# Optimization experiments

Measured on AMD Instinct MI355X. Metric: run time of the kernel, lower is better.

The kernel has to match this reference:

```python
import jax, jax.numpy as jnp
import numpy as np

N_HEAD = 16
N_KV_GROUP = 4
WINDOW = 256


def setup_inputs() -> dict:
    key = jax.random.key(0)
    ks = jax.random.split(key, 5)
    B, T, C = 2, 2048, 1024
    KV = C // N_HEAD * N_KV_GROUP  # 256
    s = 0.02
    return {
        "x": jax.random.normal(ks[0], (B, T, C), jnp.float32),
        "Wq": jax.random.normal(ks[1], (C, C), jnp.float32) * s,
        "bq": jnp.zeros((C,), jnp.float32),
        "Wk": jax.random.normal(ks[2], (C, KV), jnp.float32) * s,
        "bk": jnp.zeros((KV,), jnp.float32),
        "Wv": jax.random.normal(ks[3], (C, KV), jnp.float32) * s,
        "bv": jnp.zeros((KV,), jnp.float32),
        "Wo": jax.random.normal(ks[4], (C, C), jnp.float32) * s,
        "bo": jnp.zeros((C,), jnp.float32),
    }


def reference(x, Wq, bq, Wk, bk, Wv, bv, Wo, bo):
    B, T, C = x.shape
    hd = C // N_HEAD  # head dim = 64
    n_rep = N_HEAD // N_KV_GROUP

    q = x @ Wq + bq                      # [B,T,C]
    k = x @ Wk + bk                      # [B,T,KV]
    v = x @ Wv + bv

    q = q.reshape(B, T, N_HEAD, hd).transpose(0, 2, 1, 3)       # [B,H,T,d]
    k = k.reshape(B, T, N_KV_GROUP, hd).transpose(0, 2, 1, 3)   # [B,G,T,d]
    v = v.reshape(B, T, N_KV_GROUP, hd).transpose(0, 2, 1, 3)

    # GQA: repeat_interleave kv heads along head dim
    k_rep = jnp.repeat(k, n_rep, axis=1)                         # [B,H,T,d]
    v_rep = jnp.repeat(v, n_rep, axis=1)

    att = jnp.einsum("bhqd,bhkd->bhqk", q, k_rep) / jnp.sqrt(jnp.float32(hd))

    # causal + sliding window band mask: q position i attends to j in [i-WINDOW, i]
    i = jnp.arange(T)[:, None]
    j = jnp.arange(T)[None, :]
    band = (j <= i) & (j >= i - WINDOW)                           # [T,T]
    att = jnp.where(band[None, None], att, jnp.float32(-jnp.inf))

    att = jax.nn.softmax(att, axis=-1)
    y = jnp.einsum("bhqk,bhkd->bhqd", att, v_rep)                 # [B,H,T,d]
    y = y.transpose(0, 2, 1, 3).reshape(B, T, C)
    return y @ Wo + bo
```

## Files before the change

kernel.cpp:

```cpp
#include <hip/hip_runtime.h>
#include <hip/hip_bf16.h>

#define TT 2048
#define CC 1024
#define KVD 256
#define QKVD 1536

typedef __bf16 bf16x8 __attribute__((ext_vector_type(8)));
typedef float f32x4 __attribute__((ext_vector_type(4)));

__device__ __forceinline__ void gload_lds16(const __hip_bfloat16* g, __hip_bfloat16* l) {
  __builtin_amdgcn_global_load_lds(
      (const __attribute__((address_space(1))) unsigned int*)g,
      (__attribute__((address_space(3))) unsigned int*)l, 16, 0, 0);
}


__global__ __launch_bounds__(256) void k_convert_x(const float* __restrict__ x,
                                                   __hip_bfloat16* __restrict__ xbf) {
  size_t idx = ((size_t)blockIdx.x * 256 + threadIdx.x) * 4;
  float4 v = *(const float4*)(x + idx);
  xbf[idx + 0] = __float2bfloat16(v.x);
  xbf[idx + 1] = __float2bfloat16(v.y);
  xbf[idx + 2] = __float2bfloat16(v.z);
  xbf[idx + 3] = __float2bfloat16(v.w);
}

__global__ __launch_bounds__(256) void k_pack_w(const float* __restrict__ Wq,
                                                const float* __restrict__ Wk,
                                                const float* __restrict__ Wv,
                                                const float* __restrict__ Wo,
                                                const float* __restrict__ bq,
                                                const float* __restrict__ bk,
                                                const float* __restrict__ bv,
                                                __hip_bfloat16* __restrict__ wqkvT,
                                                __hip_bfloat16* __restrict__ woT,
                                                float* __restrict__ bqkv) {
  if (blockIdx.z == 1 && blockIdx.y >= 16) {
    if (blockIdx.y == 16 && blockIdx.x == 0) {
      for (int i = threadIdx.x; i < 1536; i += 256) {
        float v;
        if (i < 1024)      v = bq[i];
        else if (i < 1280) v = bk[i - 1024];
        else               v = bv[i - 1280];
        bqkv[i] = v;
      }
    }
    return;
  }
  __shared__ float tile[64][65];
  const int k0 = blockIdx.x * 64;
  const int n0 = blockIdx.y * 64;
  const float* src;
  int ncols;
  __hip_bfloat16* dst;
  if (blockIdx.z == 0) {
    dst = wqkvT;
    if (n0 < 1024)      { src = Wq; ncols = 1024; }
    else if (n0 < 1280) { src = Wk - 1024; ncols = 256; }
    else                { src = Wv - 1280; ncols = 256; }
  } else {
    dst = woT; src = Wo; ncols = 1024;
  }
  const int rw = threadIdx.x >> 6;
  const int cl = threadIdx.x & 63;
#pragma unroll
  for (int i = 0; i < 16; ++i) {
    const int kr = rw + i * 4;
    tile[kr][cl] = src[(size_t)(k0 + kr) * ncols + n0 + cl];
  }
  __syncthreads();
#pragma unroll
  for (int i = 0; i < 16; ++i) {
    const int nr = rw + i * 4;
    dst[(size_t)(n0 + nr) * 1024 + k0 + cl] = __float2bfloat16(tile[cl][nr]);
  }
}

__global__ __launch_bounds__(256) void k_vT(const __hip_bfloat16* __restrict__ qkv,
                                            __hip_bfloat16* __restrict__ vtg) {
  __shared__ __hip_bfloat16 tile[64][72];
  const int t0 = blockIdx.x * 64;
  const int g  = blockIdx.y;
  const int b  = blockIdx.z;
  const int r  = threadIdx.x >> 2;
  const int c  = (threadIdx.x & 3) * 16;
  const __hip_bfloat16* src = qkv + ((size_t)(b * TT + t0 + r)) * QKVD + 1280 + g * 64 + c;
  *(uint4*)&tile[r][c]     = *(const uint4*)src;
  *(uint4*)&tile[r][c + 8] = *(const uint4*)(src + 8);
  __syncthreads();
  __hip_bfloat16 tmp[16];
#pragma unroll
  for (int u = 0; u < 16; ++u) tmp[u] = tile[c + u][r];
  __hip_bfloat16* dst = vtg + ((size_t)((b * 4 + g) * 64 + r)) * TT + t0 + c;
  *(uint4*)dst       = *(const uint4*)tmp;
  *(uint4*)(dst + 8) = *(const uint4*)(tmp + 8);
}


template <bool OUT_BF16>
__global__ __launch_bounds__(256, 4) void k_gemm_bt(const __hip_bfloat16* __restrict__ A,
                                                    const __hip_bfloat16* __restrict__ BT,
                                                    const float* __restrict__ bias,
                                                    void* __restrict__ C,
                                                    int M, int N, int K) {
  __shared__ __hip_bfloat16 As[64][64];
  __shared__ __hip_bfloat16 Bs[128][64];

  const int tid  = threadIdx.x;
  const int m0   = blockIdx.y * 64;
  const int n0   = blockIdx.x * 128;
  const int w    = tid >> 6;
  const int lane = tid & 63;
  const int quad = lane >> 4;
  const int l16  = lane & 15;
  const int wm   = (w >> 1) * 32;
  const int wn   = (w & 1) * 64;

  const int dl_r = lane >> 3;
  const int dl_c = (lane & 7) ^ dl_r;

  const __hip_bfloat16* gA = A + (size_t)(m0 + w * 16 + dl_r) * K + dl_c * 8;
  const __hip_bfloat16* gB = BT + (size_t)(n0 + w * 32 + dl_r) * K + dl_c * 8;

  f32x4 acc[2][4] = {};

  const int nk = K >> 6;
  for (int kt = 0; kt < nk; ++kt) {
    const int k0 = kt << 6;
    gload_lds16(gA + k0,                 &As[w * 16][0]);
    gload_lds16(gA + k0 + (size_t)8 * K, &As[w * 16 + 8][0]);
    gload_lds16(gB + k0,                  &Bs[w * 32][0]);
    gload_lds16(gB + k0 + (size_t)8 * K,  &Bs[w * 32 + 8][0]);
    gload_lds16(gB + k0 + (size_t)16 * K, &Bs[w * 32 + 16][0]);
    gload_lds16(gB + k0 + (size_t)24 * K, &Bs[w * 32 + 24][0]);
    __syncthreads();

#pragma unroll
    for (int ks = 0; ks < 2; ++ks) {
      const int cb = (ks << 2) + quad;
      bf16x8 fa[2], fb[4];
#pragma unroll
      for (int i = 0; i < 2; ++i)
        fa[i] = *(const bf16x8*)&As[wm + i * 16 + l16][(cb ^ (l16 & 7)) << 3];
#pragma unroll
      for (int j = 0; j < 4; ++j)
        fb[j] = *(const bf16x8*)&Bs[wn + j * 16 + l16][(cb ^ (l16 & 7)) << 3];
#pragma unroll
      for (int i = 0; i < 2; ++i)
#pragma unroll
        for (int j = 0; j < 4; ++j)
          acc[i][j] = __builtin_amdgcn_mfma_f32_16x16x32_bf16(fa[i], fb[j], acc[i][j], 0, 0, 0);
    }
    __syncthreads();
  }

#pragma unroll
  for (int j = 0; j < 4; ++j) {
    const int gn = n0 + wn + j * 16 + l16;
    const float bias_v = bias[gn];
#pragma unroll
    for (int i = 0; i < 2; ++i) {
      const int gmb = m0 + wm + i * 16 + quad * 4;
#pragma unroll
      for (int r = 0; r < 4; ++r) {
        const float v = acc[i][j][r] + bias_v;
        const size_t idx = (size_t)(gmb + r) * N + gn;
        if (OUT_BF16) ((__hip_bfloat16*)C)[idx] = __float2bfloat16(v);
        else          ((float*)C)[idx] = v;
      }
    }
  }
}


__global__ __launch_bounds__(256) void k_attn(const __hip_bfloat16* __restrict__ qkv,
                                              const __hip_bfloat16* __restrict__ vtg,
                                              __hip_bfloat16* __restrict__ y) {
  __shared__ __hip_bfloat16 Ps[4][16][72];

  const int t    = threadIdx.x;
  const int w    = t >> 6;
  const int lane = t & 63;
  const int quad = lane >> 4;
  const int l16  = lane & 15;
  const int bx   = blockIdx.x;
  const int h    = blockIdx.y;
  const int b    = blockIdx.z;
  const int g    = h >> 2;
  const int i0   = bx * 64;
  const int qrow      = i0 + w * 16 + l16;
  const int my_q_base = i0 + w * 16 + quad * 4;

  bf16x8 fq[2];
  {
    const __hip_bfloat16* qp = qkv + ((size_t)(b * TT + qrow)) * QKVD + h * 64 + quad * 8;
    fq[0] = *(const bf16x8*)qp;
    fq[1] = *(const bf16x8*)(qp + 32);
  }

  float m_r[4], l_r[4];
#pragma unroll
  for (int r = 0; r < 4; ++r) { m_r[r] = -INFINITY; l_r[r] = 0.f; }
  f32x4 o_acc[4] = {};

  const int c_lo = bx >= 4 ? bx - 4 : 0;
  for (int c = c_lo; c <= bx; ++c) {
    const int jc = c * 64;

    bf16x8 fk[4][2];
    const __hip_bfloat16* kbase =
        qkv + ((size_t)(b * TT + jc + l16)) * QKVD + 1024 + g * 64 + quad * 8;
#pragma unroll
    for (int nt = 0; nt < 4; ++nt) {
      fk[nt][0] = *(const bf16x8*)(kbase + (size_t)nt * 16 * QKVD);
      fk[nt][1] = *(const bf16x8*)(kbase + (size_t)nt * 16 * QKVD + 32);
    }
    bf16x8 fv[4][2];
    const __hip_bfloat16* vbase =
        vtg + ((size_t)((b * 4 + g) * 64 + l16)) * TT + jc + quad * 8;
#pragma unroll
    for (int jt = 0; jt < 4; ++jt) {
      fv[jt][0] = *(const bf16x8*)(vbase + (size_t)jt * 16 * TT);
      fv[jt][1] = *(const bf16x8*)(vbase + (size_t)jt * 16 * TT + 32);
    }

    f32x4 sacc[4] = {};
#pragma unroll
    for (int nt = 0; nt < 4; ++nt) {
      sacc[nt] = __builtin_amdgcn_mfma_f32_16x16x32_bf16(fq[0], fk[nt][0], sacc[nt], 0, 0, 0);
      sacc[nt] = __builtin_amdgcn_mfma_f32_16x16x32_bf16(fq[1], fk[nt][1], sacc[nt], 0, 0, 0);
    }

    float alpha[4];
#pragma unroll
    for (int r = 0; r < 4; ++r) {
      const int gi = my_q_base + r;
      const int lo = gi - 256;
      float s_r[4];
      float mx = -INFINITY;
#pragma unroll
      for (int nt = 0; nt < 4; ++nt) {
        const int key = jc + nt * 16 + l16;
        float s = sacc[nt][r] * 0.125f;
        s = (key <= gi && key >= lo) ? s : -INFINITY;
        s_r[nt] = s;
        mx = fmaxf(mx, s);
      }
#pragma unroll
      for (int d = 1; d < 16; d <<= 1) mx = fmaxf(mx, __shfl_xor(mx, d));
      const float mo = m_r[r];
      const float mn = fmaxf(mo, mx);
      const float al = __expf(mo - mn);
      float sum = 0.f;
#pragma unroll
      for (int nt = 0; nt < 4; ++nt) {
        const float p = __expf(s_r[nt] - mn);
        sum += p;
        Ps[w][quad * 4 + r][nt * 16 + l16] = __float2bfloat16(p);
      }
#pragma unroll
      for (int d = 1; d < 16; d <<= 1) sum += __shfl_xor(sum, d);
      m_r[r] = mn;
      l_r[r] = l_r[r] * al + sum;
      alpha[r] = al;
    }

#pragma unroll
    for (int jt = 0; jt < 4; ++jt)
#pragma unroll
      for (int r = 0; r < 4; ++r) o_acc[jt][r] *= alpha[r];

    bf16x8 fp0 = *(const bf16x8*)&Ps[w][l16][quad * 8];
    bf16x8 fp1 = *(const bf16x8*)&Ps[w][l16][32 + quad * 8];

#pragma unroll
    for (int jt = 0; jt < 4; ++jt) {
      o_acc[jt] = __builtin_amdgcn_mfma_f32_16x16x32_bf16(fp0, fv[jt][0], o_acc[jt], 0, 0, 0);
      o_acc[jt] = __builtin_amdgcn_mfma_f32_16x16x32_bf16(fp1, fv[jt][1], o_acc[jt], 0, 0, 0);
    }
  }

#pragma unroll
  for (int r = 0; r < 4; ++r) {
    const float inv = 1.f / l_r[r];
    __hip_bfloat16* yp = y + ((size_t)(b * TT + my_q_base + r)) * CC + h * 64 + l16;
#pragma unroll
    for (int jt = 0; jt < 4; ++jt)
      yp[jt * 16] = __float2bfloat16(o_acc[jt][r] * inv);
  }
}


extern "C" void kernel_launch(void* const* d_in, const int* in_sizes, int n_in,
                              void* d_out, int out_size, void* d_ws, size_t ws_size,
                              hipStream_t stream) {
  const float* x  = (const float*)d_in[0];
  const float* Wq = (const float*)d_in[1];
  const float* bq = (const float*)d_in[2];
  const float* Wk = (const float*)d_in[3];
  const float* bk = (const float*)d_in[4];
  const float* Wv = (const float*)d_in[5];
  const float* bv = (const float*)d_in[6];
  const float* Wo = (const float*)d_in[7];
  const float* bo = (const float*)d_in[8];
  float* out = (float*)d_out;

  char* ws = (char*)d_ws;
  const size_t M = 2 * TT;
  __hip_bfloat16* xbf   = (__hip_bfloat16*)(ws);
  __hip_bfloat16* qkv   = (__hip_bfloat16*)(ws + 8388608);
  __hip_bfloat16* ybf   = (__hip_bfloat16*)(ws + 20971520);
  __hip_bfloat16* wqkvT = (__hip_bfloat16*)(ws + 29360128);
  __hip_bfloat16* woT   = (__hip_bfloat16*)(ws + 32505856);
  float*          bqkv  = (float*)(ws + 34603008);
  __hip_bfloat16* vtg   = (__hip_bfloat16*)(ws + 34609152);

  k_convert_x<<<4096, 256, 0, stream>>>(x, xbf);
  k_pack_w<<<dim3(16, 24, 2), 256, 0, stream>>>(Wq, Wk, Wv, Wo, bq, bk, bv,
                                                wqkvT, woT, bqkv);

  k_gemm_bt<true><<<dim3(QKVD / 128, M / 64), 256, 0, stream>>>(xbf, wqkvT, bqkv, qkv,
                                                                (int)M, QKVD, CC);
  k_vT<<<dim3(TT / 64, 4, 2), 256, 0, stream>>>(qkv, vtg);

  k_attn<<<dim3(TT / 64, 16, 2), 256, 0, stream>>>(qkv, vtg, ybf);

  k_gemm_bt<false><<<dim3(CC / 128, M / 64), 256, 0, stream>>>(ybf, woT, bo, out,
                                                               (int)M, CC, CC);
}
```

Before: 167.9 us.

## Split attention KV chunks across wave pairs and merge partial softmax in LDS

After: 173.7 us. 1.03x slower.

```diff
diff --git a/kernel.cpp b/kernel.cpp
--- a/kernel.cpp
+++ b/kernel.cpp
@@ -178,19 +178,23 @@
                                               const __hip_bfloat16* __restrict__ vtg,
                                               __hip_bfloat16* __restrict__ y) {
   __shared__ __hip_bfloat16 Ps[4][16][72];
+  __shared__ float Osh[2][16][72];
+  __shared__ float MLsh[2][2][16];
 
   const int t    = threadIdx.x;
   const int w    = t >> 6;
   const int lane = t & 63;
   const int quad = lane >> 4;
   const int l16  = lane & 15;
+  const int qt   = w >> 1;
+  const int sp   = w & 1;
   const int bx   = blockIdx.x;
   const int h    = blockIdx.y;
   const int b    = blockIdx.z;
   const int g    = h >> 2;
-  const int i0   = bx * 64;
-  const int qrow      = i0 + w * 16 + l16;
-  const int my_q_base = i0 + w * 16 + quad * 4;
+  const int i0   = bx * 32 + qt * 16;
+  const int qrow      = i0 + l16;
+  const int my_q_base = i0 + quad * 4;
 
   bf16x8 fq[2];
   {
@@ -204,8 +208,10 @@
   for (int r = 0; r < 4; ++r) { m_r[r] = -INFINITY; l_r[r] = 0.f; }
   f32x4 o_acc[4] = {};
 
-  const int c_lo = bx >= 4 ? bx - 4 : 0;
-  for (int c = c_lo; c <= bx; ++c) {
+  const int c_lo = (i0 >= 256) ? ((i0 - 256) >> 6) : 0;
+  const int c_hi = (i0 + 15) >> 6;
+
+  for (int c = c_lo + sp; c <= c_hi; c += 2) {
     const int jc = c * 64;
 
     bf16x8 fk[4][2];
@@ -281,13 +287,38 @@
     }
   }
 
-#pragma unroll
-  for (int r = 0; r < 4; ++r) {
-    const float inv = 1.f / l_r[r];
-    __hip_bfloat16* yp = y + ((size_t)(b * TT + my_q_base + r)) * CC + h * 64 + l16;
-#pragma unroll
-    for (int jt = 0; jt < 4; ++jt)
-      yp[jt * 16] = __float2bfloat16(o_acc[jt][r] * inv);
+  if (sp == 1) {
+#pragma unroll
+    for (int r = 0; r < 4; ++r) {
+#pragma unroll
+      for (int jt = 0; jt < 4; ++jt)
+        Osh[qt][quad * 4 + r][jt * 16 + l16] = o_acc[jt][r];
+      if (l16 == 0) {
+        MLsh[qt][0][quad * 4 + r] = m_r[r];
+        MLsh[qt][1][quad * 4 + r] = l_r[r];
+      }
+    }
+  }
+  __syncthreads();
+
+  if (sp == 0) {
+#pragma unroll
+    for (int r = 0; r < 4; ++r) {
+      const int row = quad * 4 + r;
+      const float m1 = MLsh[qt][0][row];
+      const float l1 = MLsh[qt][1][row];
+      const float m0v = m_r[r];
+      const float mm = fmaxf(m0v, m1);
+      const float a0 = __expf(m0v - mm);
+      const float a1 = __expf(m1 - mm);
+      const float inv = 1.f / (l_r[r] * a0 + l1 * a1);
+      __hip_bfloat16* yp = y + ((size_t)(b * TT + i0 + row)) * CC + h * 64 + l16;
+#pragma unroll
+      for (int jt = 0; jt < 4; ++jt) {
+        const float ov = o_acc[jt][r] * a0 + Osh[qt][row][jt * 16 + l16] * a1;
+        yp[jt * 16] = __float2bfloat16(ov * inv);
+      }
+    }
   }
 }
 
@@ -324,7 +355,7 @@
                                                                 (int)M, QKVD, CC);
   k_vT<<<dim3(TT / 64, 4, 2), 256, 0, stream>>>(qkv, vtg);
 
-  k_attn<<<dim3(TT / 64, 16, 2), 256, 0, stream>>>(qkv, vtg, ybf);
+  k_attn<<<dim3(TT / 32, 16, 2), 256, 0, stream>>>(qkv, vtg, ybf);
 
   k_gemm_bt<false><<<dim3(CC / 128, M / 64), 256, 0, stream>>>(ybf, woT, bo, out,
                                                                (int)M, CC, CC);
```
